# Kernel optimization log

Measured on AMD Instinct MI355X. Metric: run time of the kernel, lower is better.

Reference implementation:

```python
import jax, jax.numpy as jnp
import numpy as np

STRIDES = (8, 16, 32)
IMG = 1024
CENTER_RADIUS = 2.5
N_CAND = 10  # SimOTA candidate top-k


def setup_inputs() -> dict:
    key = jax.random.key(0)
    ks = jax.random.split(key, 6)
    B, G = 16, 100
    sizes = [IMG // s for s in STRIDES]
    inp = {}
    for i, H in enumerate(sizes):
        inp[f"reg{i}"] = jax.random.normal(ks[i], (B, 4, H, H), jnp.float32)
        inp[f"obj{i}"] = jax.random.normal(ks[3 + i], (B, 1, H, H), jnp.float32)
    rng = np.random.default_rng(0)
    cxy = rng.uniform(64.0, IMG - 64.0, (B, G, 2))
    wh = rng.uniform(16.0, 160.0, (B, G, 2))
    labels = np.concatenate([np.zeros((B, G, 1)), cxy, wh], axis=-1).astype(np.float32)
    counts = rng.integers(20, G + 1, B)  # variable num_gt per image, zero-padded tail
    mask = (np.arange(G)[None, :] < counts[:, None]).astype(np.float32)
    labels = labels * mask[:, :, None]
    inp["labels"] = jnp.asarray(labels)
    return inp


def _decode(regs, objs):
    outs, xs, ys, ss = [], [], [], []
    for reg, obj, s in zip(regs, objs, STRIDES):
        B, _, H, W = reg.shape
        o = jnp.concatenate([reg, obj], axis=1).transpose(0, 2, 3, 1).reshape(B, H * W, 5)
        yv, xv = jnp.meshgrid(jnp.arange(H), jnp.arange(W), indexing="ij")
        grid = jnp.stack([xv, yv], axis=-1).reshape(-1, 2).astype(o.dtype)  # [HW,2] (x,y)
        xy = (o[..., :2] + grid) * s
        wh = jnp.exp(o[..., 2:4]) * s
        outs.append(jnp.concatenate([xy, wh, o[..., 4:5]], axis=-1))
        xs.append(grid[:, 0])
        ys.append(grid[:, 1])
        ss.append(jnp.full((H * W,), float(s), o.dtype))
    return (jnp.concatenate(outs, 1), jnp.concatenate(xs), jnp.concatenate(ys), jnp.concatenate(ss))


def _pairwise_iou(gt, pr):
    # gt [G,4], pr [A,4] in cxcywh -> [G,A]
    tl = jnp.maximum(gt[:, None, :2] - gt[:, None, 2:] * 0.5, pr[None, :, :2] - pr[None, :, 2:] * 0.5)
    br = jnp.minimum(gt[:, None, :2] + gt[:, None, 2:] * 0.5, pr[None, :, :2] + pr[None, :, 2:] * 0.5)
    en = jnp.all(tl < br, axis=-1)
    area_i = jnp.prod(br - tl, axis=-1) * en
    area_g = gt[:, 2] * gt[:, 3]
    area_p = pr[:, 2] * pr[:, 3]
    return area_i / (area_g[:, None] + area_p[None, :] - area_i + 1e-16)


def _iou_loss(pred, tgt):
    # elementwise cxcywh IoU loss: 1 - iou**2 (loss_type='iou')
    tl = jnp.maximum(pred[..., :2] - pred[..., 2:] * 0.5, tgt[..., :2] - tgt[..., 2:] * 0.5)
    br = jnp.minimum(pred[..., :2] + pred[..., 2:] * 0.5, tgt[..., :2] + tgt[..., 2:] * 0.5)
    en = jnp.all(tl < br, axis=-1)
    area_i = jnp.prod(br - tl, axis=-1) * en
    area_p = pred[..., 2] * pred[..., 3]
    area_g = tgt[..., 2] * tgt[..., 3]
    iou = area_i / (area_p + area_g - area_i + 1e-16)
    return 1.0 - iou ** 2


def _assign(gt_boxes, gt_valid, bbox, obj_logit, x_c, y_c, strides):
    # SimOTA assignment for one image. gt_boxes [G,4], bbox [A,4].
    G = gt_boxes.shape[0]
    gx, gy, gw, gh = gt_boxes[:, 0], gt_boxes[:, 1], gt_boxes[:, 2], gt_boxes[:, 3]
    bl = x_c[None] - (gx - 0.5 * gw)[:, None]
    br_ = (gx + 0.5 * gw)[:, None] - x_c[None]
    bt = y_c[None] - (gy - 0.5 * gh)[:, None]
    bb = (gy + 0.5 * gh)[:, None] - y_c[None]
    in_boxes = jnp.minimum(jnp.minimum(bl, br_), jnp.minimum(bt, bb)) > 0
    r = CENTER_RADIUS * strides[None]
    cl = x_c[None] - (gx[:, None] - r)
    cr = (gx[:, None] + r) - x_c[None]
    ct = y_c[None] - (gy[:, None] - r)
    cb = (gy[:, None] + r) - y_c[None]
    in_centers = jnp.minimum(jnp.minimum(cl, cr), jnp.minimum(ct, cb)) > 0
    fg_anchor = jnp.any(in_boxes, 0) | jnp.any(in_centers, 0)
    in_both = in_boxes & in_centers

    ious = _pairwise_iou(gt_boxes, bbox)                       # [G,A]
    valid_pair = gt_valid[:, None] & fg_anchor[None, :]
    ious_m = jnp.where(valid_pair, ious, 0.0)
    obj_cost = jax.nn.softplus(-obj_logit)[None, :]            # BCE-with-logits, target=1
    cost = (obj_cost + 3.0 * (-jnp.log(ious + 1e-8))
            + 1e5 * (~in_both) + 1e7 * (~valid_pair))

    topk_ious = jax.lax.top_k(ious_m, N_CAND)[0]               # [G,10]
    dyn_k = jnp.maximum(topk_ious.sum(1).astype(jnp.int32), 1)  # dynamic k per gt
    ranks = jnp.argsort(jnp.argsort(cost, axis=1), axis=1)      # rank of each anchor per gt
    matching = (ranks < dyn_k[:, None]) & gt_valid[:, None]
    n_match = matching.sum(0)
    best_gt = jnp.argmin(cost, axis=0)                          # conflict resolution
    resolved = (jnp.arange(G)[:, None] == best_gt[None, :]) & gt_valid[:, None]
    matching = jnp.where(n_match[None, :] > 1, resolved, matching)
    fg = jnp.any(matching, 0)
    matched_gt = jnp.argmax(matching, 0)
    return fg, matched_gt, fg.sum()


def reference(reg0, reg1, reg2, obj0, obj1, obj2, labels):
    out, x_sh, y_sh, strides = _decode((reg0, reg1, reg2), (obj0, obj1, obj2))
    bbox = out[..., :4]          # [B,A,4] decoded cxcywh
    obj_logit = out[..., 4]      # [B,A]
    x_c = (x_sh + 0.5) * strides
    y_c = (y_sh + 0.5) * strides
    gt_boxes = labels[..., 1:5]
    gt_valid = labels.sum(-1) > 0
    fg, matched_gt, nfg = jax.vmap(_assign, in_axes=(0, 0, 0, 0, None, None, None))(
        gt_boxes, gt_valid, bbox, obj_logit, x_c, y_c, strides)
    num_fg = jnp.maximum(nfg.sum().astype(jnp.float32), 1.0)
    reg_tgt = jax.vmap(lambda g, i: g[i])(gt_boxes, matched_gt)  # [B,A,4]
    fgf = fg.astype(jnp.float32)
    loss_iou = (_iou_loss(bbox, reg_tgt) * fgf).sum() / num_fg
    bce = jax.nn.softplus(obj_logit) - obj_logit * fgf           # BCEWithLogits
    loss_obj = bce.sum() / num_fg
    num_gts = jnp.maximum(gt_valid.sum().astype(jnp.float32), 1.0)
    loss = 5.0 * loss_iou + loss_obj
    return (loss, 5.0 * loss_iou, loss_obj, jnp.float32(0.0), num_fg / num_gts)
```

## Files before the change

kernel.cpp:

```cpp
#include <hip/hip_runtime.h>
#include <math.h>

#define NA   21504
#define NA0  16384
#define NA01 20480
#define NG   100
#define NB   16
#define NC   10
#define NCHK 84
#define NBLK 1344
#define MAXC 192
#define MCAP 1024
#define MSTRIDE 64
#define NSQ  4

__device__ __forceinline__ float softplusf(float x) {
    return fmaxf(x, 0.f) + log1pf(expf(-fabsf(x)));
}

__device__ __forceinline__ unsigned int fmono(float f) {
    unsigned int u = __float_as_uint(f);
    return (f < 0.f) ? ~u : (u | 0x80000000u);
}

__global__ __launch_bounds__(256) void k_decode(
    const float* __restrict__ reg0, const float* __restrict__ obj0,
    const float* __restrict__ reg1, const float* __restrict__ obj1,
    const float* __restrict__ reg2, const float* __restrict__ obj2,
    const float* __restrict__ labels,
    float4* __restrict__ A0, float* __restrict__ OC,
    int* __restrict__ cidx, int* __restrict__ bcnt,
    int* __restrict__ n_match, int* __restrict__ mg_min,
    float* __restrict__ pSp, int* __restrict__ mcount,
    unsigned long long* __restrict__ bestkey, int* __restrict__ fbflag)
{
    int b  = blockIdx.y;
    int bx = blockIdx.x;
    int tid = threadIdx.x;
    int a = bx * 256 + tid;

    int W, ry0, rows; float s;
    if (bx < 64)      { W = 128; s = 8.f;  ry0 = bx * 2;        rows = 2; }
    else if (bx < 80) { W = 64;  s = 16.f; ry0 = (bx - 64) * 4; rows = 4; }
    else              { W = 32;  s = 32.f; ry0 = (bx - 80) * 8; rows = 8; }

    __shared__ unsigned int smask[8];
    if (tid < 8) smask[tid] = 0u;
    __syncthreads();

    if (tid < NG) {
        const float* L = labels + (b * NG + tid) * 5;
        float gx = L[1], gy = L[2], gw = L[3], gh = L[4];
        float r = 2.5f * s;
        float tlx = gx - 0.5f * gw, tly = gy - 0.5f * gh;
        float brx = gx + 0.5f * gw, bry = gy + 0.5f * gh;
        float cxl = gx - r, cxh = gx + r, cyl = gy - r, cyh = gy + r;
        float lox = fminf(tlx, cxl), hix = fmaxf(brx, cxh);
        float loy = fminf(tly, cyl), hiy = fmaxf(bry, cyh);
        int ixA = (int)floorf(lox / s - 0.5f) - 1;
        int ixB = (int)ceilf (hix / s - 0.5f) + 1;
        int iyA = (int)floorf(loy / s - 0.5f) - 1;
        int iyB = (int)ceilf (hiy / s - 0.5f) + 1;
        ixA = max(ixA, 0); ixB = min(ixB, W - 1);
        iyA = max(iyA, ry0); iyB = min(iyB, ry0 + rows - 1);
        for (int iy = iyA; iy <= iyB; iy++) {
            float yc = ((float)iy + 0.5f) * s;
            float mb = fminf(yc - tly, bry - yc);
            float mc = fminf(yc - cyl, cyh - yc);
            for (int ix = ixA; ix <= ixB; ix++) {
                float xc = ((float)ix + 0.5f) * s;
                bool inb = fminf(fminf(xc - tlx, brx - xc), mb) > 0.f;
                bool inc = fminf(fminf(xc - cxl, cxh - xc), mc) > 0.f;
                if (inb || inc) {
                    int bit = (iy - ry0) * W + ix;
                    atomicOr(&smask[bit >> 5], 1u << (bit & 31));
                }
            }
        }
    }

    int x, y, hw, loc;
    const float* regp; const float* objp;
    if (a < NA0)       { x = a & 127;           y = a >> 7; hw = 16384; loc = y * 128 + x; regp = reg0; objp = obj0; }
    else if (a < NA01) { int i = a - NA0;  x = i & 63; y = i >> 6; hw = 4096;  loc = y * 64 + x;  regp = reg1; objp = obj1; }
    else               { int i = a - NA01; x = i & 31; y = i >> 5; hw = 1024;  loc = y * 32 + x;  regp = reg2; objp = obj2; }

    float r0 = regp[(b * 4 + 0) * hw + loc];
    float r1 = regp[(b * 4 + 1) * hw + loc];
    float r2 = regp[(b * 4 + 2) * hw + loc];
    float r3 = regp[(b * 4 + 3) * hw + loc];
    float ol = objp[b * hw + loc];

    float px = (r0 + (float)x) * s, py = (r1 + (float)y) * s;
    float pw = expf(r2) * s,        ph = expf(r3) * s;
    float ocv = softplusf(-ol);

    int idx = b * NA + a;
    A0[idx] = make_float4(px - 0.5f * pw, py - 0.5f * ph, px + 0.5f * pw, py + 0.5f * ph);
    OC[idx] = ocv;
    n_match[idx] = 0;
    mg_min[idx]  = 0x7fffffff;
    bestkey[idx] = 0xFFFFFFFFFFFFFFFFull;

    __syncthreads();
    bool fga = (smask[tid >> 5] >> (tid & 31)) & 1u;

    float sp = ocv + ol;
    for (int off = 32; off > 0; off >>= 1) sp += __shfl_down(sp, off);

    unsigned long long mask = __ballot(fga);
    int lane = tid & 63, wid = tid >> 6;
    __shared__ float wSp[4];
    __shared__ int   wcnt[4];
    if (lane == 0) { wSp[wid] = sp; wcnt[wid] = __popcll(mask); }
    __syncthreads();
    int wbase = 0;
    #pragma unroll
    for (int w2 = 0; w2 < 4; w2++) if (w2 < wid) wbase += wcnt[w2];
    if (fga) {
        int prefix = __popcll(mask & ((1ull << lane) - 1ull));
        cidx[b * NA + bx * 256 + wbase + prefix] = a;
    }
    if (tid == 0) {
        bcnt[b * NCHK + bx] = wcnt[0] + wcnt[1] + wcnt[2] + wcnt[3];
        pSp[b * NCHK + bx]  = wSp[0] + wSp[1] + wSp[2] + wSp[3];
        if (bx == 0) { mcount[b * MSTRIDE] = 0; fbflag[b] = 0; }
    }
}

__global__ __launch_bounds__(256) void k_pack(
    const float4* __restrict__ A0, const float* __restrict__ OC,
    const int* __restrict__ cidx, const int* __restrict__ bcnt,
    float4* __restrict__ PK0, float* __restrict__ PKO, int* __restrict__ PKA,
    int* __restrict__ fcnt)
{
    int b = blockIdx.y, bx = blockIdx.x, tid = threadIdx.x;
    int v = 0;
    for (int i = tid; i < bx; i += 256) v += bcnt[b * NCHK + i];
    for (int off = 32; off > 0; off >>= 1) v += __shfl_down(v, off);
    __shared__ int ws[4];
    int wid = tid >> 6;
    if ((tid & 63) == 0) ws[wid] = v;
    __syncthreads();
    int base = ws[0] + ws[1] + ws[2] + ws[3];
    int nt = bcnt[b * NCHK + bx];
    if (tid < nt) {
        int a = cidx[b * NA + bx * 256 + tid];
        int idx = b * NA + a;
        int d = b * NA + base + tid;
        PK0[d] = A0[idx];
        PKO[d] = OC[idx];
        PKA[d] = a;
    }
    if (bx == NCHK - 1 && tid == 0) fcnt[b] = base + nt;
}

__global__ __launch_bounds__(256) void k_assign(
    const float* __restrict__ labels, const float4* __restrict__ A0,
    const float* __restrict__ OC,
    const float4* __restrict__ PK0, const float* __restrict__ PKO,
    const int* __restrict__ PKA, const int* __restrict__ fcnt,
    int* __restrict__ n_match, int* __restrict__ mg_min,
    int* __restrict__ mlist, int* __restrict__ mcount,
    unsigned long long* __restrict__ bestkey, int* __restrict__ fbflag)
{
    int blk = blockIdx.x;
    int b = blk / NG, g = blk % NG;
    const float* L = labels + (b * NG + g) * 5;
    float l0 = L[0], gx = L[1], gy = L[2], gw = L[3], gh = L[4];
    bool gv = (l0 + gx + gy + gw + gh) > 0.f;
    if (!gv) return;
    int tid = threadIdx.x;

    float g_tlx = gx - 0.5f * gw, g_tly = gy - 0.5f * gh;
    float g_brx = gx + 0.5f * gw, g_bry = gy + 0.5f * gh;
    float ag = gw * gh;
    int bbase = b * NA;

    __shared__ float sio[256 * NC];
    __shared__ int   si2[256 * NC];
    __shared__ int   cand_a[MAXC];
    __shared__ float cand_c[MAXC];
    __shared__ int   scnt;
    if (tid == 0) scnt = 0;
    __syncthreads();

    int cnt = fcnt[b];

    float tio[NC];
    #pragma unroll
    for (int k = 0; k < NC; k++) tio[k] = 0.f;

    for (int m = tid; m < cnt; m += 256) {
        float4 c0 = PK0[bbase + m];
        float pa = (c0.z - c0.x) * (c0.w - c0.y);
        float tlx = fmaxf(g_tlx, c0.x), tly = fmaxf(g_tly, c0.y);
        float brx = fminf(g_brx, c0.z), bry = fminf(g_bry, c0.w);
        bool en = (tlx < brx) && (tly < bry);
        float ai = en ? (brx - tlx) * (bry - tly) : 0.f;
        float iou = ai / (ag + pa - ai + 1e-16f);
        if (iou > tio[NC - 1]) {
            tio[NC - 1] = iou;
            #pragma unroll
            for (int j = NC - 1; j > 0; --j) {
                if (tio[j] > tio[j - 1]) { float t = tio[j]; tio[j] = tio[j - 1]; tio[j - 1] = t; }
            }
        }
    }

    #pragma unroll
    for (int k = 0; k < NC; k++) sio[tid * NC + k] = tio[k];
    __syncthreads();

    for (int off = 128; off > 0; off >>= 1) {
        if (tid < off) {
            int abase = tid * NC, bb2 = (tid + off) * NC;
            int i = 0, j = 0;
            float oo_[NC];
            #pragma unroll
            for (int k = 0; k < NC; k++) {
                float va = sio[abase + i], vb = sio[bb2 + j];
                bool ta = va >= vb;
                oo_[k] = ta ? va : vb;
                i += ta ? 1 : 0; j += ta ? 0 : 1;
            }
            #pragma unroll
            for (int k = 0; k < NC; k++) sio[abase + k] = oo_[k];
        }
        __syncthreads();
    }

    float s10 = 0.f;
    #pragma unroll
    for (int k = 0; k < NC; k++) s10 += sio[k];
    int dk = (int)s10;
    if (dk < 1) dk = 1;
    if (dk > NC) dk = NC;

    for (int lev = 0; lev < 3; lev++) {
        float s  = (lev == 0) ? 8.f : ((lev == 1) ? 16.f : 32.f);
        int   W  = (lev == 0) ? 128 : ((lev == 1) ? 64 : 32);
        int aofs = (lev == 0) ? 0 : ((lev == 1) ? NA0 : NA01);
        float rr = 2.5f * s;
        float gxr_lo = gx - rr, gxr_hi = gx + rr;
        float gyr_lo = gy - rr, gyr_hi = gy + rr;
        float lox = fmaxf(g_tlx, gxr_lo), hix = fminf(g_brx, gxr_hi);
        float loy = fmaxf(g_tly, gyr_lo), hiy = fminf(g_bry, gyr_hi);
        int ixA = (int)floorf(lox / s - 0.5f) - 1;
        int ixB = (int)ceilf (hix / s - 0.5f) + 1;
        int iyA = (int)floorf(loy / s - 0.5f) - 1;
        int iyB = (int)ceilf (hiy / s - 0.5f) + 1;
        ixA = max(ixA, 0); ixB = min(ixB, W - 1);
        iyA = max(iyA, 0); iyB = min(iyB, W - 1);
        int nx = ixB - ixA + 1, ny = iyB - iyA + 1;
        int nt = (nx > 0 && ny > 0) ? nx * ny : 0;
        for (int t = tid; t < nt; t += 256) {
            int ix = ixA + t % nx, iy = iyA + t / nx;
            float xcA = ((float)ix + 0.5f) * s;
            float ycA = ((float)iy + 0.5f) * s;
            float bl = xcA - g_tlx, brr = g_brx - xcA;
            float bt = ycA - g_tly, bbb = g_bry - ycA;
            bool inb = fminf(fminf(bl, brr), fminf(bt, bbb)) > 0.f;
            float cl = xcA - gxr_lo, cr = gxr_hi - xcA;
            float ct = ycA - gyr_lo, cb = gyr_hi - ycA;
            bool inc = fminf(fminf(cl, cr), fminf(ct, cb)) > 0.f;
            if (inb && inc) {
                int p = atomicAdd(&scnt, 1);
                if (p < MAXC) cand_a[p] = aofs + iy * W + ix;
            }
        }
    }
    __syncthreads();
    int nc_ = min(scnt, MAXC);

    if (dk <= nc_) {
        for (int ci = tid; ci < nc_; ci += 256) {
            int a = cand_a[ci];
            float4 c0 = A0[bbase + a];
            float pa = (c0.z - c0.x) * (c0.w - c0.y);
            float tlx = fmaxf(g_tlx, c0.x), tly = fmaxf(g_tly, c0.y);
            float brx = fminf(g_brx, c0.z), bry = fminf(g_bry, c0.w);
            bool en = (tlx < brx) && (tly < bry);
            float ai = en ? (brx - tlx) * (bry - tly) : 0.f;
            float iou = ai / (ag + pa - ai + 1e-16f);
            float c = OC[bbase + a] + 3.0f * (-__logf(iou + 1e-8f));
            cand_c[ci] = c;
            unsigned long long key = ((unsigned long long)fmono(c) << 32) | (unsigned int)g;
            atomicMin(&bestkey[bbase + a], key);
        }
        __syncthreads();
        for (int ci = tid; ci < nc_; ci += 256) {
            float c = cand_c[ci]; int a = cand_a[ci];
            int rank = 0;
            for (int j = 0; j < nc_; j++) {
                float cj = cand_c[j]; int aj = cand_a[j];
                rank += (cj < c || (cj == c && aj < a)) ? 1 : 0;
            }
            if (rank < dk) {
                if (atomicAdd(&n_match[bbase + a], 1) == 0) {
                    int p = atomicAdd(&mcount[b * MSTRIDE], 1);
                    mlist[b * MCAP + p] = a;
                }
                atomicMin(&mg_min[bbase + a], g);
            }
        }
    } else {
        if (tid == 0) fbflag[b] = 1;
        float fc[NC]; int fa[NC];
        #pragma unroll
        for (int k = 0; k < NC; k++) { fc[k] = 3.4e38f; fa[k] = 0x7fffffff; }
        for (int m = tid; m < cnt; m += 256) {
            int a = PKA[bbase + m];
            float4 c0 = PK0[bbase + m];
            float pa = (c0.z - c0.x) * (c0.w - c0.y);
            float tlx = fmaxf(g_tlx, c0.x), tly = fmaxf(g_tly, c0.y);
            float brx = fminf(g_brx, c0.z), bry = fminf(g_bry, c0.w);
            bool en = (tlx < brx) && (tly < bry);
            float ai = en ? (brx - tlx) * (bry - tly) : 0.f;
            float iou = ai / (ag + pa - ai + 1e-16f);
            int xx, yy; float s2;
            if (a < NA0)       { xx = a & 127;           yy = a >> 7;  s2 = 8.f;  }
            else if (a < NA01) { int i2 = a - NA0;  xx = i2 & 63; yy = i2 >> 6; s2 = 16.f; }
            else               { int i2 = a - NA01; xx = i2 & 31; yy = i2 >> 5; s2 = 32.f; }
            float xcA = ((float)xx + 0.5f) * s2, ycA = ((float)yy + 0.5f) * s2;
            float rr2 = 2.5f * s2;
            float bl = xcA - g_tlx, brr = g_brx - xcA;
            float bt = ycA - g_tly, bbb = g_bry - ycA;
            bool inb = fminf(fminf(bl, brr), fminf(bt, bbb)) > 0.f;
            float cl = xcA - (gx - rr2), cr = (gx + rr2) - xcA;
            float ct = ycA - (gy - rr2), cb = (gy + rr2) - ycA;
            bool inc = fminf(fminf(cl, cr), fminf(ct, cb)) > 0.f;
            float c = PKO[bbase + m] + 3.0f * (-__logf(iou + 1e-8f));
            if (!(inb && inc)) c += 100000.0f;
            if (c < fc[NC - 1] || (c == fc[NC - 1] && a < fa[NC - 1])) {
                fc[NC - 1] = c; fa[NC - 1] = a;
                #pragma unroll
                for (int j = NC - 1; j > 0; --j) {
                    bool sw = (fc[j] < fc[j - 1]) || (fc[j] == fc[j - 1] && fa[j] < fa[j - 1]);
                    if (sw) {
                        float t1 = fc[j]; fc[j] = fc[j - 1]; fc[j - 1] = t1;
                        int   t2 = fa[j]; fa[j] = fa[j - 1]; fa[j - 1] = t2;
                    }
                }
            }
        }
        __syncthreads();
        #pragma unroll
        for (int k = 0; k < NC; k++) { sio[tid * NC + k] = fc[k]; si2[tid * NC + k] = fa[k]; }
        __syncthreads();
        for (int off = 128; off > 0; off >>= 1) {
            if (tid < off) {
                int abase = tid * NC, bb2 = (tid + off) * NC;
                int i = 0, j = 0;
                float oc_[NC]; int oi_[NC];
                #pragma unroll
                for (int k = 0; k < NC; k++) {
                    float ca = sio[abase + i], cb3 = sio[bb2 + j];
                    int   ia = si2[abase + i], ib  = si2[bb2 + j];
                    bool ta = (ca < cb3) || (ca == cb3 && ia <= ib);
                    oc_[k] = ta ? ca : cb3; oi_[k] = ta ? ia : ib;
                    i += ta ? 1 : 0; j += ta ? 0 : 1;
                }
                #pragma unroll
                for (int k = 0; k < NC; k++) { sio[abase + k] = oc_[k]; si2[abase + k] = oi_[k]; }
            }
            __syncthreads();
        }
        if (tid == 0) {
            for (int k = 0; k < dk; k++) {
                int aa = si2[k];
                if (aa != 0x7fffffff) {
                    if (atomicAdd(&n_match[bbase + aa], 1) == 0) {
                        int p = atomicAdd(&mcount[b * MSTRIDE], 1);
                        mlist[b * MCAP + p] = aa;
                    }
                    atomicMin(&mg_min[bbase + aa], g);
                }
            }
        }
    }
}

__global__ __launch_bounds__(256) void k_sparse(
    const float* __restrict__ labels,
    const float* __restrict__ obj0, const float* __restrict__ obj1,
    const float* __restrict__ obj2,
    const float4* __restrict__ A0, const float* __restrict__ OC,
    const int* __restrict__ n_match, const int* __restrict__ mg_min,
    const int* __restrict__ mlist, const int* __restrict__ mcount,
    const unsigned long long* __restrict__ bestkey, const int* __restrict__ fbflag,
    float* __restrict__ pIl2, float* __restrict__ pOl, int* __restrict__ pNf2)
{
    int q = blockIdx.x;
    int b = blockIdx.y;
    int tid = threadIdx.x;
    __shared__ float lbl[NG * 5];
    for (int i = tid; i < NG * 5; i += 256) lbl[i] = labels[b * NG * 5 + i];
    __syncthreads();

    int cm = min(mcount[b * MSTRIDE], MCAP);
    int fb = fbflag[b];
    float il_s = 0.f, ol_s = 0.f; int nf = 0;

    for (int m = q * 256 + tid; m < cm; m += NSQ * 256) {
        int a = mlist[b * MCAP + m];
        int idx = b * NA + a;
        int n = n_match[idx];

        int x, y, hw, loc; const float* objp; float s, rr;
        if (a < NA0)       { x = a & 127;            y = a >> 7;  hw = 16384; loc = y * 128 + x; objp = obj0; s = 8.f;  rr = 20.f; }
        else if (a < NA01) { int i2 = a - NA0;  x = i2 & 63; y = i2 >> 6; hw = 4096; loc = y * 64 + x; objp = obj1; s = 16.f; rr = 40.f; }
        else               { int i2 = a - NA01; x = i2 & 31; y = i2 >> 5; hw = 1024; loc = y * 32 + x; objp = obj2; s = 32.f; rr = 80.f; }

        float4 c0 = A0[idx];
        bool fg = false; int mg = 0;
        if (n == 1) { fg = true; mg = mg_min[idx]; }
        else {
            unsigned long long key = fb ? 0xFFFFFFFFFFFFFFFFull : bestkey[idx];
            if (key != 0xFFFFFFFFFFFFFFFFull) {
                fg = true; mg = (int)(key & 0xFFFFFFFFull);
            } else {
                float pa = (c0.z - c0.x) * (c0.w - c0.y);
                float oc = OC[idx];
                float xcA = ((float)x + 0.5f) * s, ycA = ((float)y + 0.5f) * s;
                float bestc = 3.4e38f; int bg = 0;
                for (int g = 0; g < NG; g++) {
                    float l0 = lbl[g * 5 + 0], gx = lbl[g * 5 + 1], gy = lbl[g * 5 + 2];
                    float gw = lbl[g * 5 + 3], gh = lbl[g * 5 + 4];
                    bool gvv = (l0 + gx + gy + gw + gh) > 0.f;
                    float tlx = fmaxf(gx - 0.5f * gw, c0.x), tly = fmaxf(gy - 0.5f * gh, c0.y);
                    float brx = fminf(gx + 0.5f * gw, c0.z), bry = fminf(gy + 0.5f * gh, c0.w);
                    bool en = (tlx < brx) && (tly < bry);
                    float ai = en ? (brx - tlx) * (bry - tly) : 0.f;
                    float iou = ai / (gw * gh + pa - ai + 1e-16f);
                    float bl = xcA - (gx - 0.5f * gw), br = (gx + 0.5f * gw) - xcA;
                    float bt = ycA - (gy - 0.5f * gh), bb = (gy + 0.5f * gh) - ycA;
                    bool inb = fminf(fminf(bl, br), fminf(bt, bb)) > 0.f;
                    float cl = xcA - (gx - rr), cr = (gx + rr) - xcA;
                    float ct = ycA - (gy - rr), cb = (gy + rr) - ycA;
                    bool inc = fminf(fminf(cl, cr), fminf(ct, cb)) > 0.f;
                    float c = oc + 3.0f * (-__logf(iou + 1e-8f));
                    if (!(inb && inc)) c += 100000.0f;
                    if (!gvv)          c += 10000000.0f;
                    if (c < bestc) { bestc = c; bg = g; }
                }
                bool gvv = (lbl[bg * 5 + 0] + lbl[bg * 5 + 1] + lbl[bg * 5 + 2] +
                            lbl[bg * 5 + 3] + lbl[bg * 5 + 4]) > 0.f;
                if (gvv) { fg = true; mg = bg; }
            }
        }

        if (fg) {
            float pa = (c0.z - c0.x) * (c0.w - c0.y);
            float gx = lbl[mg * 5 + 1], gy = lbl[mg * 5 + 2];
            float gw = lbl[mg * 5 + 3], gh = lbl[mg * 5 + 4];
            float tlx = fmaxf(c0.x, gx - 0.5f * gw);
            float tly = fmaxf(c0.y, gy - 0.5f * gh);
            float brx = fminf(c0.z, gx + 0.5f * gw);
            float bry = fminf(c0.w, gy + 0.5f * gh);
            bool en = (tlx < brx) && (tly < bry);
            float ai = en ? (brx - tlx) * (bry - tly) : 0.f;
            float iou = ai / (pa + gw * gh - ai + 1e-16f);
            il_s += 1.f - iou * iou;
            ol_s += objp[b * hw + loc];
            nf++;
        }
    }

    for (int off = 32; off > 0; off >>= 1) {
        il_s += __shfl_down(il_s, off);
        ol_s += __shfl_down(ol_s, off);
        nf   += __shfl_down(nf, off);
    }
    __shared__ float wI[4], wO[4];
    __shared__ int   wN[4];
    int wid = tid >> 6;
    if ((tid & 63) == 0) { wI[wid] = il_s; wO[wid] = ol_s; wN[wid] = nf; }
    __syncthreads();
    if (tid == 0) {
        int pb = b * NSQ + q;
        pIl2[pb] = wI[0] + wI[1] + wI[2] + wI[3];
        pOl[pb]  = wO[0] + wO[1] + wO[2] + wO[3];
        pNf2[pb] = wN[0] + wN[1] + wN[2] + wN[3];
    }
}

__global__ __launch_bounds__(256) void k_fin(
    const float* __restrict__ pSp, const float* __restrict__ pIl2,
    const float* __restrict__ pOl, const int* __restrict__ pNf2,
    const float* __restrict__ labels, float* __restrict__ out)
{
    int tid = threadIdx.x;
    double dSp = 0.0;
    for (int i = tid; i < NBLK; i += 256) dSp += (double)pSp[i];
    double dIl = 0.0, dOl = 0.0; int nf = 0;
    for (int i = tid; i < NB * NSQ; i += 256) {
        dIl += (double)pIl2[i];
        dOl += (double)pOl[i];
        nf  += pNf2[i];
    }
    int ng = 0;
    for (int i = tid; i < NB * NG; i += 256) {
        const float* L = labels + i * 5;
        if (L[0] + L[1] + L[2] + L[3] + L[4] > 0.f) ng++;
    }
    for (int off = 32; off > 0; off >>= 1) {
        dSp += __shfl_down(dSp, off);
        dIl += __shfl_down(dIl, off);
        dOl += __shfl_down(dOl, off);
        nf  += __shfl_down(nf, off);
        ng  += __shfl_down(ng, off);
    }
    __shared__ double sSp[4], sIl[4], sOl[4];
    __shared__ int sNf[4], sNg[4];
    int wid = tid >> 6;
    if ((tid & 63) == 0) { sSp[wid] = dSp; sIl[wid] = dIl; sOl[wid] = dOl; sNf[wid] = nf; sNg[wid] = ng; }
    __syncthreads();
    if (tid == 0) {
        double tSp = sSp[0] + sSp[1] + sSp[2] + sSp[3];
        double tIl = sIl[0] + sIl[1] + sIl[2] + sIl[3];
        double tOl = sOl[0] + sOl[1] + sOl[2] + sOl[3];
        int tNf = sNf[0] + sNf[1] + sNf[2] + sNf[3];
        int tNg = sNg[0] + sNg[1] + sNg[2] + sNg[3];
        float num_fg  = fmaxf((float)tNf, 1.f);
        float num_gts = fmaxf((float)tNg, 1.f);
        float li = (float)(tIl / (double)num_fg);
        float lo = (float)((tSp - tOl) / (double)num_fg);
        out[0] = 5.f * li + lo;
        out[1] = 5.f * li;
        out[2] = lo;
        out[3] = 0.f;
        out[4] = num_fg / num_gts;
    }
}

extern "C" void kernel_launch(void* const* d_in, const int* in_sizes, int n_in,
                              void* d_out, int out_size, void* d_ws, size_t ws_size,
                              hipStream_t stream)
{
    const float* reg0   = (const float*)d_in[0];
    const float* obj0   = (const float*)d_in[1];
    const float* reg1   = (const float*)d_in[2];
    const float* obj1   = (const float*)d_in[3];
    const float* reg2   = (const float*)d_in[4];
    const float* obj2   = (const float*)d_in[5];
    const float* labels = (const float*)d_in[6];
    float* out = (float*)d_out;

    char* w = (char*)d_ws;
    size_t off = 0;
    int*    mcount = (int*)(w + off);     off += (size_t)NB * MSTRIDE * 4;
    int*    bcnt   = (int*)(w + off);     off += (size_t)NB * NCHK * 4;
    int*    fcnt   = (int*)(w + off);     off += (size_t)NB * 4;
    int*    fbflag = (int*)(w + off);     off += (size_t)NB * 4;
    float*  pSp    = (float*)(w + off);   off += (size_t)NBLK * 4;
    float*  pIl2   = (float*)(w + off);   off += (size_t)NB * NSQ * 4;
    float*  pOl    = (float*)(w + off);   off += (size_t)NB * NSQ * 4;
    int*    pNf2   = (int*)(w + off);     off += (size_t)NB * NSQ * 4;
    off = (off + 255) & ~(size_t)255;
    float4* A0      = (float4*)(w + off); off += (size_t)NB * NA * 16;
    float4* PK0     = (float4*)(w + off); off += (size_t)NB * NA * 16;
    unsigned long long* bestkey = (unsigned long long*)(w + off); off += (size_t)NB * NA * 8;
    float*  OC      = (float*)(w + off);  off += (size_t)NB * NA * 4;
    float*  PKO     = (float*)(w + off);  off += (size_t)NB * NA * 4;
    int*    PKA     = (int*)(w + off);    off += (size_t)NB * NA * 4;
    int*    cidx    = (int*)(w + off);    off += (size_t)NB * NA * 4;
    int*    n_match = (int*)(w + off);    off += (size_t)NB * NA * 4;
    int*    mg_min  = (int*)(w + off);    off += (size_t)NB * NA * 4;
    int*    mlist   = (int*)(w + off);    off += (size_t)NB * MCAP * 4;

    dim3 gA(NCHK, NB);

    k_decode<<<gA, 256, 0, stream>>>(reg0, obj0, reg1, obj1, reg2, obj2, labels,
                                     A0, OC, cidx, bcnt, n_match, mg_min, pSp, mcount,
                                     bestkey, fbflag);
    k_pack<<<gA, 256, 0, stream>>>(A0, OC, cidx, bcnt, PK0, PKO, PKA, fcnt);
    k_assign<<<dim3(NB * NG), 256, 0, stream>>>(labels, A0, OC, PK0, PKO, PKA, fcnt,
                                                n_match, mg_min, mlist, mcount,
                                                bestkey, fbflag);
    k_sparse<<<dim3(NSQ, NB), 256, 0, stream>>>(labels, obj0, obj1, obj2, A0, OC,
                                                n_match, mg_min, mlist, mcount,
                                                bestkey, fbflag, pIl2, pOl, pNf2);
    k_fin<<<1, 256, 0, stream>>>(pSp, pIl2, pOl, pNf2, labels, out);
}
```

Baseline: 123.8 us.

## Fuse sparse loss and final reduction into assign kernel via last-block counters

Folds the k_sparse and k_fin stages into k_assign. Per-image done counters let the last gt block of each image run the loss accumulation, and a global counter lets the last image block compute the final output. Decode now writes boxes and objectness cost only for anchors that pass the centre/box prefilter, and the per-anchor state initialisation moves into the pack kernel, which only touches candidate anchors. The aim is to cut two kernel launches and a large share of global writes. In exchange it adds a memset, atomic fences and serial tail work on one block per image.

```diff
diff --git a/kernel.cpp b/kernel.cpp
--- a/kernel.cpp
+++ b/kernel.cpp
@@ -12,7 +12,7 @@
 #define MAXC 192
 #define MCAP 1024
 #define MSTRIDE 64
-#define NSQ  4
+#define DSTRIDE 64
 
 __device__ __forceinline__ float softplusf(float x) {
     return fmaxf(x, 0.f) + log1pf(expf(-fabsf(x)));
@@ -30,9 +30,7 @@
     const float* __restrict__ labels,
     float4* __restrict__ A0, float* __restrict__ OC,
     int* __restrict__ cidx, int* __restrict__ bcnt,
-    int* __restrict__ n_match, int* __restrict__ mg_min,
-    float* __restrict__ pSp, int* __restrict__ mcount,
-    unsigned long long* __restrict__ bestkey, int* __restrict__ fbflag)
+    float* __restrict__ pSp)
 {
     int b  = blockIdx.y;
     int bx = blockIdx.x;
@@ -95,15 +93,14 @@
     float pw = expf(r2) * s,        ph = expf(r3) * s;
     float ocv = softplusf(-ol);
 
-    int idx = b * NA + a;
-    A0[idx] = make_float4(px - 0.5f * pw, py - 0.5f * ph, px + 0.5f * pw, py + 0.5f * ph);
-    OC[idx] = ocv;
-    n_match[idx] = 0;
-    mg_min[idx]  = 0x7fffffff;
-    bestkey[idx] = 0xFFFFFFFFFFFFFFFFull;
-
     __syncthreads();
     bool fga = (smask[tid >> 5] >> (tid & 31)) & 1u;
+
+    int idx = b * NA + a;
+    if (fga) {
+        A0[idx] = make_float4(px - 0.5f * pw, py - 0.5f * ph, px + 0.5f * pw, py + 0.5f * ph);
+        OC[idx] = ocv;
+    }
 
     float sp = ocv + ol;
     for (int off = 32; off > 0; off >>= 1) sp += __shfl_down(sp, off);
@@ -124,7 +121,6 @@
     if (tid == 0) {
         bcnt[b * NCHK + bx] = wcnt[0] + wcnt[1] + wcnt[2] + wcnt[3];
         pSp[b * NCHK + bx]  = wSp[0] + wSp[1] + wSp[2] + wSp[3];
-        if (bx == 0) { mcount[b * MSTRIDE] = 0; fbflag[b] = 0; }
     }
 }
 
@@ -132,7 +128,10 @@
     const float4* __restrict__ A0, const float* __restrict__ OC,
     const int* __restrict__ cidx, const int* __restrict__ bcnt,
     float4* __restrict__ PK0, float* __restrict__ PKO, int* __restrict__ PKA,
-    int* __restrict__ fcnt)
+    int* __restrict__ fcnt,
+    int* __restrict__ n_match, int* __restrict__ mg_min,
+    unsigned long long* __restrict__ bestkey,
+    int* __restrict__ mcount, int* __restrict__ fbflag)
 {
     int b = blockIdx.y, bx = blockIdx.x, tid = threadIdx.x;
     int v = 0;
@@ -151,166 +150,59 @@
         PK0[d] = A0[idx];
         PKO[d] = OC[idx];
         PKA[d] = a;
+        n_match[idx] = 0;
+        mg_min[idx]  = 0x7fffffff;
+        bestkey[idx] = 0xFFFFFFFFFFFFFFFFull;
     }
     if (bx == NCHK - 1 && tid == 0) fcnt[b] = base + nt;
+    if (bx == 0 && tid == 0) { mcount[b * MSTRIDE] = 0; fbflag[b] = 0; }
 }
 
 __global__ __launch_bounds__(256) void k_assign(
     const float* __restrict__ labels, const float4* __restrict__ A0,
     const float* __restrict__ OC,
+    const float* __restrict__ obj0, const float* __restrict__ obj1,
+    const float* __restrict__ obj2,
     const float4* __restrict__ PK0, const float* __restrict__ PKO,
     const int* __restrict__ PKA, const int* __restrict__ fcnt,
     int* __restrict__ n_match, int* __restrict__ mg_min,
     int* __restrict__ mlist, int* __restrict__ mcount,
-    unsigned long long* __restrict__ bestkey, int* __restrict__ fbflag)
+    unsigned long long* __restrict__ bestkey, int* __restrict__ fbflag,
+    const float* __restrict__ pSp,
+    float* __restrict__ pIl2, float* __restrict__ pOl, int* __restrict__ pNf2,
+    int* __restrict__ doneA, int* __restrict__ gdone,
+    float* __restrict__ out)
 {
     int blk = blockIdx.x;
     int b = blk / NG, g = blk % NG;
-    const float* L = labels + (b * NG + g) * 5;
-    float l0 = L[0], gx = L[1], gy = L[2], gw = L[3], gh = L[4];
-    bool gv = (l0 + gx + gy + gw + gh) > 0.f;
-    if (!gv) return;
     int tid = threadIdx.x;
-
-    float g_tlx = gx - 0.5f * gw, g_tly = gy - 0.5f * gh;
-    float g_brx = gx + 0.5f * gw, g_bry = gy + 0.5f * gh;
-    float ag = gw * gh;
-    int bbase = b * NA;
 
     __shared__ float sio[256 * NC];
     __shared__ int   si2[256 * NC];
     __shared__ int   cand_a[MAXC];
     __shared__ float cand_c[MAXC];
     __shared__ int   scnt;
-    if (tid == 0) scnt = 0;
-    __syncthreads();
-
-    int cnt = fcnt[b];
-
-    float tio[NC];
-    #pragma unroll
-    for (int k = 0; k < NC; k++) tio[k] = 0.f;
-
-    for (int m = tid; m < cnt; m += 256) {
-        float4 c0 = PK0[bbase + m];
-        float pa = (c0.z - c0.x) * (c0.w - c0.y);
-        float tlx = fmaxf(g_tlx, c0.x), tly = fmaxf(g_tly, c0.y);
-        float brx = fminf(g_brx, c0.z), bry = fminf(g_bry, c0.w);
-        bool en = (tlx < brx) && (tly < bry);
-        float ai = en ? (brx - tlx) * (bry - tly) : 0.f;
-        float iou = ai / (ag + pa - ai + 1e-16f);
-        if (iou > tio[NC - 1]) {
-            tio[NC - 1] = iou;
-            #pragma unroll
-            for (int j = NC - 1; j > 0; --j) {
-                if (tio[j] > tio[j - 1]) { float t = tio[j]; tio[j] = tio[j - 1]; tio[j - 1] = t; }
-            }
-        }
-    }
-
-    #pragma unroll
-    for (int k = 0; k < NC; k++) sio[tid * NC + k] = tio[k];
-    __syncthreads();
-
-    for (int off = 128; off > 0; off >>= 1) {
-        if (tid < off) {
-            int abase = tid * NC, bb2 = (tid + off) * NC;
-            int i = 0, j = 0;
-            float oo_[NC];
-            #pragma unroll
-            for (int k = 0; k < NC; k++) {
-                float va = sio[abase + i], vb = sio[bb2 + j];
-                bool ta = va >= vb;
-                oo_[k] = ta ? va : vb;
-                i += ta ? 1 : 0; j += ta ? 0 : 1;
-            }
-            #pragma unroll
-            for (int k = 0; k < NC; k++) sio[abase + k] = oo_[k];
-        }
+    __shared__ int   s_t, s_g;
+
+    const float* L = labels + (b * NG + g) * 5;
+    float l0 = L[0], gx = L[1], gy = L[2], gw = L[3], gh = L[4];
+    bool gv = (l0 + gx + gy + gw + gh) > 0.f;
+    int bbase = b * NA;
+
+    if (gv) {
+        float g_tlx = gx - 0.5f * gw, g_tly = gy - 0.5f * gh;
+        float g_brx = gx + 0.5f * gw, g_bry = gy + 0.5f * gh;
+        float ag = gw * gh;
+        if (tid == 0) scnt = 0;
         __syncthreads();
-    }
-
-    float s10 = 0.f;
-    #pragma unroll
-    for (int k = 0; k < NC; k++) s10 += sio[k];
-    int dk = (int)s10;
-    if (dk < 1) dk = 1;
-    if (dk > NC) dk = NC;
-
-    for (int lev = 0; lev < 3; lev++) {
-        float s  = (lev == 0) ? 8.f : ((lev == 1) ? 16.f : 32.f);
-        int   W  = (lev == 0) ? 128 : ((lev == 1) ? 64 : 32);
-        int aofs = (lev == 0) ? 0 : ((lev == 1) ? NA0 : NA01);
-        float rr = 2.5f * s;
-        float gxr_lo = gx - rr, gxr_hi = gx + rr;
-        float gyr_lo = gy - rr, gyr_hi = gy + rr;
-        float lox = fmaxf(g_tlx, gxr_lo), hix = fminf(g_brx, gxr_hi);
-        float loy = fmaxf(g_tly, gyr_lo), hiy = fminf(g_bry, gyr_hi);
-        int ixA = (int)floorf(lox / s - 0.5f) - 1;
-        int ixB = (int)ceilf (hix / s - 0.5f) + 1;
-        int iyA = (int)floorf(loy / s - 0.5f) - 1;
-        int iyB = (int)ceilf (hiy / s - 0.5f) + 1;
-        ixA = max(ixA, 0); ixB = min(ixB, W - 1);
-        iyA = max(iyA, 0); iyB = min(iyB, W - 1);
-        int nx = ixB - ixA + 1, ny = iyB - iyA + 1;
-        int nt = (nx > 0 && ny > 0) ? nx * ny : 0;
-        for (int t = tid; t < nt; t += 256) {
-            int ix = ixA + t % nx, iy = iyA + t / nx;
-            float xcA = ((float)ix + 0.5f) * s;
-            float ycA = ((float)iy + 0.5f) * s;
-            float bl = xcA - g_tlx, brr = g_brx - xcA;
-            float bt = ycA - g_tly, bbb = g_bry - ycA;
-            bool inb = fminf(fminf(bl, brr), fminf(bt, bbb)) > 0.f;
-            float cl = xcA - gxr_lo, cr = gxr_hi - xcA;
-            float ct = ycA - gyr_lo, cb = gyr_hi - ycA;
-            bool inc = fminf(fminf(cl, cr), fminf(ct, cb)) > 0.f;
-            if (inb && inc) {
-                int p = atomicAdd(&scnt, 1);
-                if (p < MAXC) cand_a[p] = aofs + iy * W + ix;
-            }
-        }
-    }
-    __syncthreads();
-    int nc_ = min(scnt, MAXC);
-
-    if (dk <= nc_) {
-        for (int ci = tid; ci < nc_; ci += 256) {
-            int a = cand_a[ci];
-            float4 c0 = A0[bbase + a];
-            float pa = (c0.z - c0.x) * (c0.w - c0.y);
-            float tlx = fmaxf(g_tlx, c0.x), tly = fmaxf(g_tly, c0.y);
-            float brx = fminf(g_brx, c0.z), bry = fminf(g_bry, c0.w);
-            bool en = (tlx < brx) && (tly < bry);
-            float ai = en ? (brx - tlx) * (bry - tly) : 0.f;
-            float iou = ai / (ag + pa - ai + 1e-16f);
-            float c = OC[bbase + a] + 3.0f * (-__logf(iou + 1e-8f));
-            cand_c[ci] = c;
-            unsigned long long key = ((unsigned long long)fmono(c) << 32) | (unsigned int)g;
-            atomicMin(&bestkey[bbase + a], key);
-        }
-        __syncthreads();
-        for (int ci = tid; ci < nc_; ci += 256) {
-            float c = cand_c[ci]; int a = cand_a[ci];
-            int rank = 0;
-            for (int j = 0; j < nc_; j++) {
-                float cj = cand_c[j]; int aj = cand_a[j];
-                rank += (cj < c || (cj == c && aj < a)) ? 1 : 0;
-            }
-            if (rank < dk) {
-                if (atomicAdd(&n_match[bbase + a], 1) == 0) {
-                    int p = atomicAdd(&mcount[b * MSTRIDE], 1);
-                    mlist[b * MCAP + p] = a;
-                }
-                atomicMin(&mg_min[bbase + a], g);
-            }
-        }
-    } else {
-        if (tid == 0) fbflag[b] = 1;
-        float fc[NC]; int fa[NC];
+
+        int cnt = fcnt[b];
+
+        float tio[NC];
         #pragma unroll
-        for (int k = 0; k < NC; k++) { fc[k] = 3.4e38f; fa[k] = 0x7fffffff; }
+        for (int k = 0; k < NC; k++) tio[k] = 0.f;
+
         for (int m = tid; m < cnt; m += 256) {
-            int a = PKA[bbase + m];
             float4 c0 = PK0[bbase + m];
             float pa = (c0.z - c0.x) * (c0.w - c0.y);
             float tlx = fmaxf(g_tlx, c0.x), tly = fmaxf(g_tly, c0.y);
@@ -318,219 +210,329 @@
             bool en = (tlx < brx) && (tly < bry);
             float ai = en ? (brx - tlx) * (bry - tly) : 0.f;
             float iou = ai / (ag + pa - ai + 1e-16f);
-            int xx, yy; float s2;
-            if (a < NA0)       { xx = a & 127;           yy = a >> 7;  s2 = 8.f;  }
-            else if (a < NA01) { int i2 = a - NA0;  xx = i2 & 63; yy = i2 >> 6; s2 = 16.f; }
-            else               { int i2 = a - NA01; xx = i2 & 31; yy = i2 >> 5; s2 = 32.f; }
-            float xcA = ((float)xx + 0.5f) * s2, ycA = ((float)yy + 0.5f) * s2;
-            float rr2 = 2.5f * s2;
-            float bl = xcA - g_tlx, brr = g_brx - xcA;
-            float bt = ycA - g_tly, bbb = g_bry - ycA;
-            bool inb = fminf(fminf(bl, brr), fminf(bt, bbb)) > 0.f;
-            float cl = xcA - (gx - rr2), cr = (gx + rr2) - xcA;
-            float ct = ycA - (gy - rr2), cb = (gy + rr2) - ycA;
-            bool inc = fminf(fminf(cl, cr), fminf(ct, cb)) > 0.f;
-            float c = PKO[bbase + m] + 3.0f * (-__logf(iou + 1e-8f));
-            if (!(inb && inc)) c += 100000.0f;
-            if (c < fc[NC - 1] || (c == fc[NC - 1] && a < fa[NC - 1])) {
-                fc[NC - 1] = c; fa[NC - 1] = a;
+            if (iou > tio[NC - 1]) {
+                tio[NC - 1] = iou;
                 #pragma unroll
                 for (int j = NC - 1; j > 0; --j) {
-                    bool sw = (fc[j] < fc[j - 1]) || (fc[j] == fc[j - 1] && fa[j] < fa[j - 1]);
-                    if (sw) {
-                        float t1 = fc[j]; fc[j] = fc[j - 1]; fc[j - 1] = t1;
-                        int   t2 = fa[j]; fa[j] = fa[j - 1]; fa[j - 1] = t2;
-                    }
-                }
-            }
-        }
+                    if (tio[j] > tio[j - 1]) { float t = tio[j]; tio[j] = tio[j - 1]; tio[j - 1] = t; }
+                }
+            }
+        }
+
+        #pragma unroll
+        for (int k = 0; k < NC; k++) sio[tid * NC + k] = tio[k];
         __syncthreads();
-        #pragma unroll
-        for (int k = 0; k < NC; k++) { sio[tid * NC + k] = fc[k]; si2[tid * NC + k] = fa[k]; }
-        __syncthreads();
+
         for (int off = 128; off > 0; off >>= 1) {
             if (tid < off) {
                 int abase = tid * NC, bb2 = (tid + off) * NC;
                 int i = 0, j = 0;
-                float oc_[NC]; int oi_[NC];
+                float oo_[NC];
                 #pragma unroll
                 for (int k = 0; k < NC; k++) {
-                    float ca = sio[abase + i], cb3 = sio[bb2 + j];
-                    int   ia = si2[abase + i], ib  = si2[bb2 + j];
-                    bool ta = (ca < cb3) || (ca == cb3 && ia <= ib);
-                    oc_[k] = ta ? ca : cb3; oi_[k] = ta ? ia : ib;
+                    float va = sio[abase + i], vb = sio[bb2 + j];
+                    bool ta = va >= vb;
+                    oo_[k] = ta ? va : vb;
                     i += ta ? 1 : 0; j += ta ? 0 : 1;
                 }
                 #pragma unroll
-                for (int k = 0; k < NC; k++) { sio[abase + k] = oc_[k]; si2[abase + k] = oi_[k]; }
+                for (int k = 0; k < NC; k++) sio[abase + k] = oo_[k];
             }
             __syncthreads();
         }
+
+        float s10 = 0.f;
+        #pragma unroll
+        for (int k = 0; k < NC; k++) s10 += sio[k];
+        int dk = (int)s10;
+        if (dk < 1) dk = 1;
+        if (dk > NC) dk = NC;
+
+        for (int lev = 0; lev < 3; lev++) {
+            float s  = (lev == 0) ? 8.f : ((lev == 1) ? 16.f : 32.f);
+            int   W  = (lev == 0) ? 128 : ((lev == 1) ? 64 : 32);
+            int aofs = (lev == 0) ? 0 : ((lev == 1) ? NA0 : NA01);
+            float rr = 2.5f * s;
+            float gxr_lo = gx - rr, gxr_hi = gx + rr;
+            float gyr_lo = gy - rr, gyr_hi = gy + rr;
+            float lox = fmaxf(g_tlx, gxr_lo), hix = fminf(g_brx, gxr_hi);
+            float loy = fmaxf(g_tly, gyr_lo), hiy = fminf(g_bry, gyr_hi);
+            int ixA = (int)floorf(lox / s - 0.5f) - 1;
+            int ixB = (int)ceilf (hix / s - 0.5f) + 1;
+            int iyA = (int)floorf(loy / s - 0.5f) - 1;
+            int iyB = (int)ceilf (hiy / s - 0.5f) + 1;
+            ixA = max(ixA, 0); ixB = min(ixB, W - 1);
+            iyA = max(iyA, 0); iyB = min(iyB, W - 1);
+            int nx = ixB - ixA + 1, ny = iyB - iyA + 1;
+            int nt = (nx > 0 && ny > 0) ? nx * ny : 0;
+            for (int t = tid; t < nt; t += 256) {
+                int ix = ixA + t % nx, iy = iyA + t / nx;
+                float xcA = ((float)ix + 0.5f) * s;
+                float ycA = ((float)iy + 0.5f) * s;
+                float bl = xcA - g_tlx, brr = g_brx - xcA;
+                float bt = ycA - g_tly, bbb = g_bry - ycA;
+                bool inb = fminf(fminf(bl, brr), fminf(bt, bbb)) > 0.f;
+                float cl = xcA - gxr_lo, cr = gxr_hi - xcA;
+                float ct = ycA - gyr_lo, cb = gyr_hi - ycA;
+                bool inc = fminf(fminf(cl, cr), fminf(ct, cb)) > 0.f;
+                if (inb && inc) {
+                    int p = atomicAdd(&scnt, 1);
+                    if (p < MAXC) cand_a[p] = aofs + iy * W + ix;
+                }
+            }
+        }
+        __syncthreads();
+        int nc_ = min(scnt, MAXC);
+
+        if (dk <= nc_) {
+            for (int ci = tid; ci < nc_; ci += 256) {
+                int a = cand_a[ci];
+                float4 c0 = A0[bbase + a];
+                float pa = (c0.z - c0.x) * (c0.w - c0.y);
+                float tlx = fmaxf(g_tlx, c0.x), tly = fmaxf(g_tly, c0.y);
+                float brx = fminf(g_brx, c0.z), bry = fminf(g_bry, c0.w);
+                bool en = (tlx < brx) && (tly < bry);
+                float ai = en ? (brx - tlx) * (bry - tly) : 0.f;
+                float iou = ai / (ag + pa - ai + 1e-16f);
+                float c = OC[bbase + a] + 3.0f * (-__logf(iou + 1e-8f));
+                cand_c[ci] = c;
+                unsigned long long key = ((unsigned long long)fmono(c) << 32) | (unsigned int)g;
+                atomicMin(&bestkey[bbase + a], key);
+            }
+            __syncthreads();
+            for (int ci = tid; ci < nc_; ci += 256) {
+                float c = cand_c[ci]; int a = cand_a[ci];
+                int rank = 0;
+                for (int j = 0; j < nc_; j++) {
+                    float cj = cand_c[j]; int aj = cand_a[j];
+                    rank += (cj < c || (cj == c && aj < a)) ? 1 : 0;
+                }
+                if (rank < dk) {
+                    if (atomicAdd(&n_match[bbase + a], 1) == 0) {
+                        int p = atomicAdd(&mcount[b * MSTRIDE], 1);
+                        atomicExch(&mlist[b * MCAP + p], a);
+                    }
+                    atomicMin(&mg_min[bbase + a], g);
+                }
+            }
+        } else {
+            if (tid == 0) atomicExch(&fbflag[b], 1);
+            int cnt2 = cnt;
+            float fc[NC]; int fa[NC];
+            #pragma unroll
+            for (int k = 0; k < NC; k++) { fc[k] = 3.4e38f; fa[k] = 0x7fffffff; }
+            for (int m = tid; m < cnt2; m += 256) {
+                int a = PKA[bbase + m];
+                float4 c0 = PK0[bbase + m];
+                float pa = (c0.z - c0.x) * (c0.w - c0.y);
+                float tlx = fmaxf(g_tlx, c0.x), tly = fmaxf(g_tly, c0.y);
+                float brx = fminf(g_brx, c0.z), bry = fminf(g_bry, c0.w);
+                bool en = (tlx < brx) && (tly < bry);
+                float ai = en ? (brx - tlx) * (bry - tly) : 0.f;
+                float iou = ai / (ag + pa - ai + 1e-16f);
+                int xx, yy; float s2;
+                if (a < NA0)       { xx = a & 127;           yy = a >> 7;  s2 = 8.f;  }
+                else if (a < NA01) { int i2 = a - NA0;  xx = i2 & 63; yy = i2 >> 6; s2 = 16.f; }
+                else               { int i2 = a - NA01; xx = i2 & 31; yy = i2 >> 5; s2 = 32.f; }
+                float xcA = ((float)xx + 0.5f) * s2, ycA = ((float)yy + 0.5f) * s2;
+                float rr2 = 2.5f * s2;
+                float bl = xcA - g_tlx, brr = g_brx - xcA;
+                float bt = ycA - g_tly, bbb = g_bry - ycA;
+                bool inb = fminf(fminf(bl, brr), fminf(bt, bbb)) > 0.f;
+                float cl = xcA - (gx - rr2), cr = (gx + rr2) - xcA;
+                float ct = ycA - (gy - rr2), cb = (gy + rr2) - ycA;
+                bool inc = fminf(fminf(cl, cr), fminf(ct, cb)) > 0.f;
+                float c = PKO[bbase + m] + 3.0f * (-__logf(iou + 1e-8f));
+                if (!(inb && inc)) c += 100000.0f;
+                if (c < fc[NC - 1] || (c == fc[NC - 1] && a < fa[NC - 1])) {
+                    fc[NC - 1] = c; fa[NC - 1] = a;
+                    #pragma unroll
+                    for (int j = NC - 1; j > 0; --j) {
+                        bool sw = (fc[j] < fc[j - 1]) || (fc[j] == fc[j - 1] && fa[j] < fa[j - 1]);
+                        if (sw) {
+                            float t1 = fc[j]; fc[j] = fc[j - 1]; fc[j - 1] = t1;
+                            int   t2 = fa[j]; fa[j] = fa[j - 1]; fa[j - 1] = t2;
+                        }
+                    }
+                }
+            }
+            __syncthreads();
+            #pragma unroll
+            for (int k = 0; k < NC; k++) { sio[tid * NC + k] = fc[k]; si2[tid * NC + k] = fa[k]; }
+            __syncthreads();
+            for (int off = 128; off > 0; off >>= 1) {
+                if (tid < off) {
+                    int abase = tid * NC, bb2 = (tid + off) * NC;
+                    int i = 0, j = 0;
+                    float oc_[NC]; int oi_[NC];
+                    #pragma unroll
+                    for (int k = 0; k < NC; k++) {
+                        float ca = sio[abase + i], cb3 = sio[bb2 + j];
+                        int   ia = si2[abase + i], ib  = si2[bb2 + j];
+                        bool ta = (ca < cb3) || (ca == cb3 && ia <= ib);
+                        oc_[k] = ta ? ca : cb3; oi_[k] = ta ? ia : ib;
+                        i += ta ? 1 : 0; j += ta ? 0 : 1;
+                    }
+                    #pragma unroll
+                    for (int k = 0; k < NC; k++) { sio[abase + k] = oc_[k]; si2[abase + k] = oi_[k]; }
+                }
+                __syncthreads();
+            }
+            if (tid == 0) {
+                for (int k = 0; k < dk; k++) {
+                    int aa = si2[k];
+                    if (aa != 0x7fffffff) {
+                        if (atomicAdd(&n_match[bbase + aa], 1) == 0) {
+                            int p = atomicAdd(&mcount[b * MSTRIDE], 1);
+                            atomicExch(&mlist[b * MCAP + p], aa);
+                        }
+                        atomicMin(&mg_min[bbase + aa], g);
+                    }
+                }
+            }
+        }
+    }
+
+    __syncthreads();
+    if (tid == 0) s_t = atomicAdd(&doneA[b * DSTRIDE], 1);
+    __syncthreads();
+    if (s_t == NG - 1) {
+        __threadfence();
+        float* lbl = sio;
+        for (int i = tid; i < NG * 5; i += 256) lbl[i] = labels[b * NG * 5 + i];
+        __syncthreads();
+
+        int cm = min(mcount[b * MSTRIDE], MCAP);
+        int fb = fbflag[b];
+        float il_s = 0.f, ol_s = 0.f; int nf = 0;
+
+        for (int m = tid; m < cm; m += 256) {
+            int a = mlist[b * MCAP + m];
+            int idx = bbase + a;
+            int n = n_match[idx];
+
+            int x, y, hw, loc; const float* objp; float s, rr;
+            if (a < NA0)       { x = a & 127;            y = a >> 7;  hw = 16384; loc = y * 128 + x; objp = obj0; s = 8.f;  rr = 20.f; }
+            else if (a < NA01) { int i2 = a - NA0;  x = i2 & 63; y = i2 >> 6; hw = 4096; loc = y * 64 + x; objp = obj1; s = 16.f; rr = 40.f; }
+            else               { int i2 = a - NA01; x = i2 & 31; y = i2 >> 5; hw = 1024; loc = y * 32 + x; objp = obj2; s = 32.f; rr = 80.f; }
+
+            float4 c0 = A0[idx];
+            bool fg = false; int mg = 0;
+            if (n == 1) { fg = true; mg = mg_min[idx]; }
+            else {
+                unsigned long long key = fb ? 0xFFFFFFFFFFFFFFFFull : bestkey[idx];
+                if (key != 0xFFFFFFFFFFFFFFFFull) {
+                    fg = true; mg = (int)(key & 0xFFFFFFFFull);
+                } else {
+                    float pa = (c0.z - c0.x) * (c0.w - c0.y);
+                    float oc = OC[idx];
+                    float xcA = ((float)x + 0.5f) * s, ycA = ((float)y + 0.5f) * s;
+                    float bestc = 3.4e38f; int bg = 0;
+                    for (int g2 = 0; g2 < NG; g2++) {
+                        float l02 = lbl[g2 * 5 + 0], gx2 = lbl[g2 * 5 + 1], gy2 = lbl[g2 * 5 + 2];
+                        float gw2 = lbl[g2 * 5 + 3], gh2 = lbl[g2 * 5 + 4];
+                        bool gvv = (l02 + gx2 + gy2 + gw2 + gh2) > 0.f;
+                        float tlx = fmaxf(gx2 - 0.5f * gw2, c0.x), tly = fmaxf(gy2 - 0.5f * gh2, c0.y);
+                        float brx = fminf(gx2 + 0.5f * gw2, c0.z), bry = fminf(gy2 + 0.5f * gh2, c0.w);
+                        bool en = (tlx < brx) && (tly < bry);
+                        float ai = en ? (brx - tlx) * (bry - tly) : 0.f;
+                        float iou = ai / (gw2 * gh2 + pa - ai + 1e-16f);
+                        float bl = xcA - (gx2 - 0.5f * gw2), br = (gx2 + 0.5f * gw2) - xcA;
+                        float bt = ycA - (gy2 - 0.5f * gh2), bb = (gy2 + 0.5f * gh2) - ycA;
+                        bool inb = fminf(fminf(bl, br), fminf(bt, bb)) > 0.f;
+                        float cl = xcA - (gx2 - rr), cr = (gx2 + rr) - xcA;
+                        float ct = ycA - (gy2 - rr), cb = (gy2 + rr) - ycA;
+                        bool inc = fminf(fminf(cl, cr), fminf(ct, cb)) > 0.f;
+                        float c = oc + 3.0f * (-__logf(iou + 1e-8f));
+                        if (!(inb && inc)) c += 100000.0f;
+                        if (!gvv)          c += 10000000.0f;
+                        if (c < bestc) { bestc = c; bg = g2; }
+                    }
+                    bool gvv = (lbl[bg * 5 + 0] + lbl[bg * 5 + 1] + lbl[bg * 5 + 2] +
+                                lbl[bg * 5 + 3] + lbl[bg * 5 + 4]) > 0.f;
+                    if (gvv) { fg = true; mg = bg; }
+                }
+            }
+
+            if (fg) {
+                float pa = (c0.z - c0.x) * (c0.w - c0.y);
+                float gx2 = lbl[mg * 5 + 1], gy2 = lbl[mg * 5 + 2];
+                float gw2 = lbl[mg * 5 + 3], gh2 = lbl[mg * 5 + 4];
+                float tlx = fmaxf(c0.x, gx2 - 0.5f * gw2);
+                float tly = fmaxf(c0.y, gy2 - 0.5f * gh2);
+                float brx = fminf(c0.z, gx2 + 0.5f * gw2);
+                float bry = fminf(c0.w, gy2 + 0.5f * gh2);
+                bool en = (tlx < brx) && (tly < bry);
+                float ai = en ? (brx - tlx) * (bry - tly) : 0.f;
+                float iou = ai / (pa + gw2 * gh2 - ai + 1e-16f);
+                il_s += 1.f - iou * iou;
+                ol_s += objp[b * hw + loc];
+                nf++;
+            }
+        }
+
+        for (int off = 32; off > 0; off >>= 1) {
+            il_s += __shfl_down(il_s, off);
+            ol_s += __shfl_down(ol_s, off);
+            nf   += __shfl_down(nf, off);
+        }
+        __shared__ float wI[4], wO[4];
+        __shared__ int   wN[4];
+        int wid = tid >> 6;
+        if ((tid & 63) == 0) { wI[wid] = il_s; wO[wid] = ol_s; wN[wid] = nf; }
+        __syncthreads();
         if (tid == 0) {
-            for (int k = 0; k < dk; k++) {
-                int aa = si2[k];
-                if (aa != 0x7fffffff) {
-                    if (atomicAdd(&n_match[bbase + aa], 1) == 0) {
-                        int p = atomicAdd(&mcount[b * MSTRIDE], 1);
-                        mlist[b * MCAP + p] = aa;
-                    }
-                    atomicMin(&mg_min[bbase + aa], g);
-                }
-            }
-        }
-    }
-}
-
-__global__ __launch_bounds__(256) void k_sparse(
-    const float* __restrict__ labels,
-    const float* __restrict__ obj0, const float* __restrict__ obj1,
-    const float* __restrict__ obj2,
-    const float4* __restrict__ A0, const float* __restrict__ OC,
-    const int* __restrict__ n_match, const int* __restrict__ mg_min,
-    const int* __restrict__ mlist, const int* __restrict__ mcount,
-    const unsigned long long* __restrict__ bestkey, const int* __restrict__ fbflag,
-    float* __restrict__ pIl2, float* __restrict__ pOl, int* __restrict__ pNf2)
-{
-    int q = blockIdx.x;
-    int b = blockIdx.y;
-    int tid = threadIdx.x;
-    __shared__ float lbl[NG * 5];
-    for (int i = tid; i < NG * 5; i += 256) lbl[i] = labels[b * NG * 5 + i];
-    __syncthreads();
-
-    int cm = min(mcount[b * MSTRIDE], MCAP);
-    int fb = fbflag[b];
-    float il_s = 0.f, ol_s = 0.f; int nf = 0;
-
-    for (int m = q * 256 + tid; m < cm; m += NSQ * 256) {
-        int a = mlist[b * MCAP + m];
-        int idx = b * NA + a;
-        int n = n_match[idx];
-
-        int x, y, hw, loc; const float* objp; float s, rr;
-        if (a < NA0)       { x = a & 127;            y = a >> 7;  hw = 16384; loc = y * 128 + x; objp = obj0; s = 8.f;  rr = 20.f; }
-        else if (a < NA01) { int i2 = a - NA0;  x = i2 & 63; y = i2 >> 6; hw = 4096; loc = y * 64 + x; objp = obj1; s = 16.f; rr = 40.f; }
-        else               { int i2 = a - NA01; x = i2 & 31; y = i2 >> 5; hw = 1024; loc = y * 32 + x; objp = obj2; s = 32.f; rr = 80.f; }
-
-        float4 c0 = A0[idx];
-        bool fg = false; int mg = 0;
-        if (n == 1) { fg = true; mg = mg_min[idx]; }
-        else {
-            unsigned long long key = fb ? 0xFFFFFFFFFFFFFFFFull : bestkey[idx];
-            if (key != 0xFFFFFFFFFFFFFFFFull) {
-                fg = true; mg = (int)(key & 0xFFFFFFFFull);
-            } else {
-                float pa = (c0.z - c0.x) * (c0.w - c0.y);
-                float oc = OC[idx];
-                float xcA = ((float)x + 0.5f) * s, ycA = ((float)y + 0.5f) * s;
-                float bestc = 3.4e38f; int bg = 0;
-                for (int g = 0; g < NG; g++) {
-                    float l0 = lbl[g * 5 + 0], gx = lbl[g * 5 + 1], gy = lbl[g * 5 + 2];
-                    float gw = lbl[g * 5 + 3], gh = lbl[g * 5 + 4];
-                    bool gvv = (l0 + gx + gy + gw + gh) > 0.f;
-                    float tlx = fmaxf(gx - 0.5f * gw, c0.x), tly = fmaxf(gy - 0.5f * gh, c0.y);
-                    float brx = fminf(gx + 0.5f * gw, c0.z), bry = fminf(gy + 0.5f * gh, c0.w);
-                    bool en = (tlx < brx) && (tly < bry);
-                    float ai = en ? (brx - tlx) * (bry - tly) : 0.f;
-                    float iou = ai / (gw * gh + pa - ai + 1e-16f);
-                    float bl = xcA - (gx - 0.5f * gw), br = (gx + 0.5f * gw) - xcA;
-                    float bt = ycA - (gy - 0.5f * gh), bb = (gy + 0.5f * gh) - ycA;
-                    bool inb = fminf(fminf(bl, br), fminf(bt, bb)) > 0.f;
-                    float cl = xcA - (gx - rr), cr = (gx + rr) - xcA;
-                    float ct = ycA - (gy - rr), cb = (gy + rr) - ycA;
-                    bool inc = fminf(fminf(cl, cr), fminf(ct, cb)) > 0.f;
-                    float c = oc + 3.0f * (-__logf(iou + 1e-8f));
-                    if (!(inb && inc)) c += 100000.0f;
-                    if (!gvv)          c += 10000000.0f;
-                    if (c < bestc) { bestc = c; bg = g; }
-                }
-                bool gvv = (lbl[bg * 5 + 0] + lbl[bg * 5 + 1] + lbl[bg * 5 + 2] +
-                            lbl[bg * 5 + 3] + lbl[bg * 5 + 4]) > 0.f;
-                if (gvv) { fg = true; mg = bg; }
-            }
-        }
-
-        if (fg) {
-            float pa = (c0.z - c0.x) * (c0.w - c0.y);
-            float gx = lbl[mg * 5 + 1], gy = lbl[mg * 5 + 2];
-            float gw = lbl[mg * 5 + 3], gh = lbl[mg * 5 + 4];
-            float tlx = fmaxf(c0.x, gx - 0.5f * gw);
-            float tly = fmaxf(c0.y, gy - 0.5f * gh);
-            float brx = fminf(c0.z, gx + 0.5f * gw);
-            float bry = fminf(c0.w, gy + 0.5f * gh);
-            bool en = (tlx < brx) && (tly < bry);
-            float ai = en ? (brx - tlx) * (bry - tly) : 0.f;
-            float iou = ai / (pa + gw * gh - ai + 1e-16f);
-            il_s += 1.f - iou * iou;
-            ol_s += objp[b * hw + loc];
-            nf++;
-        }
-    }
-
-    for (int off = 32; off > 0; off >>= 1) {
-        il_s += __shfl_down(il_s, off);
-        ol_s += __shfl_down(ol_s, off);
-        nf   += __shfl_down(nf, off);
-    }
-    __shared__ float wI[4], wO[4];
-    __shared__ int   wN[4];
-    int wid = tid >> 6;
-    if ((tid & 63) == 0) { wI[wid] = il_s; wO[wid] = ol_s; wN[wid] = nf; }
-    __syncthreads();
-    if (tid == 0) {
-        int pb = b * NSQ + q;
-        pIl2[pb] = wI[0] + wI[1] + wI[2] + wI[3];
-        pOl[pb]  = wO[0] + wO[1] + wO[2] + wO[3];
-        pNf2[pb] = wN[0] + wN[1] + wN[2] + wN[3];
-    }
-}
-
-__global__ __launch_bounds__(256) void k_fin(
-    const float* __restrict__ pSp, const float* __restrict__ pIl2,
-    const float* __restrict__ pOl, const int* __restrict__ pNf2,
-    const float* __restrict__ labels, float* __restrict__ out)
-{
-    int tid = threadIdx.x;
-    double dSp = 0.0;
-    for (int i = tid; i < NBLK; i += 256) dSp += (double)pSp[i];
-    double dIl = 0.0, dOl = 0.0; int nf = 0;
-    for (int i = tid; i < NB * NSQ; i += 256) {
-        dIl += (double)pIl2[i];
-        dOl += (double)pOl[i];
-        nf  += pNf2[i];
-    }
-    int ng = 0;
-    for (int i = tid; i < NB * NG; i += 256) {
-        const float* L = labels + i * 5;
-        if (L[0] + L[1] + L[2] + L[3] + L[4] > 0.f) ng++;
-    }
-    for (int off = 32; off > 0; off >>= 1) {
-        dSp += __shfl_down(dSp, off);
-        dIl += __shfl_down(dIl, off);
-        dOl += __shfl_down(dOl, off);
-        nf  += __shfl_down(nf, off);
-        ng  += __shfl_down(ng, off);
-    }
-    __shared__ double sSp[4], sIl[4], sOl[4];
-    __shared__ int sNf[4], sNg[4];
-    int wid = tid >> 6;
-    if ((tid & 63) == 0) { sSp[wid] = dSp; sIl[wid] = dIl; sOl[wid] = dOl; sNf[wid] = nf; sNg[wid] = ng; }
-    __syncthreads();
-    if (tid == 0) {
-        double tSp = sSp[0] + sSp[1] + sSp[2] + sSp[3];
-        double tIl = sIl[0] + sIl[1] + sIl[2] + sIl[3];
-        double tOl = sOl[0] + sOl[1] + sOl[2] + sOl[3];
-        int tNf = sNf[0] + sNf[1] + sNf[2] + sNf[3];
-        int tNg = sNg[0] + sNg[1] + sNg[2] + sNg[3];
-        float num_fg  = fmaxf((float)tNf, 1.f);
-        float num_gts = fmaxf((float)tNg, 1.f);
-        float li = (float)(tIl / (double)num_fg);
-        float lo = (float)((tSp - tOl) / (double)num_fg);
-        out[0] = 5.f * li + lo;
-        out[1] = 5.f * li;
-        out[2] = lo;
-        out[3] = 0.f;
-        out[4] = num_fg / num_gts;
+            pIl2[b] = wI[0] + wI[1] + wI[2] + wI[3];
+            pOl[b]  = wO[0] + wO[1] + wO[2] + wO[3];
+            pNf2[b] = wN[0] + wN[1] + wN[2] + wN[3];
+            __threadfence();
+            s_g = atomicAdd(gdone, 1);
+        }
+        __syncthreads();
+
+        if (s_g == NB - 1) {
+            __threadfence();
+            double dSp = 0.0;
+            for (int i = tid; i < NBLK; i += 256) dSp += (double)pSp[i];
+            double dIl = 0.0, dOl = 0.0; int nf2 = 0;
+            if (tid < NB) {
+                dIl = (double)pIl2[tid];
+                dOl = (double)pOl[tid];
+                nf2 = pNf2[tid];
+            }
+            int ng = 0;
+            for (int i = tid; i < NB * NG; i += 256) {
+                const float* L2 = labels + i * 5;
+                if (L2[0] + L2[1] + L2[2] + L2[3] + L2[4] > 0.f) ng++;
+            }
+            for (int off = 32; off > 0; off >>= 1) {
+                dSp += __shfl_down(dSp, off);
+                dIl += __shfl_down(dIl, off);
+                dOl += __shfl_down(dOl, off);
+                nf2 += __shfl_down(nf2, off);
+                ng  += __shfl_down(ng, off);
+            }
+            __shared__ double fSp[4], fIl[4], fOl[4];
+            __shared__ int fNf[4], fNg[4];
+            if ((tid & 63) == 0) { fSp[wid] = dSp; fIl[wid] = dIl; fOl[wid] = dOl; fNf[wid] = nf2; fNg[wid] = ng; }
+            __syncthreads();
+            if (tid == 0) {
+                double tSp = fSp[0] + fSp[1] + fSp[2] + fSp[3];
+                double tIl = fIl[0] + fIl[1] + fIl[2] + fIl[3];
+                double tOl = fOl[0] + fOl[1] + fOl[2] + fOl[3];
+                int tNf = fNf[0] + fNf[1] + fNf[2] + fNf[3];
+                int tNg = fNg[0] + fNg[1] + fNg[2] + fNg[3];
+                float num_fg  = fmaxf((float)tNf, 1.f);
+                float num_gts = fmaxf((float)tNg, 1.f);
+                float li = (float)(tIl / (double)num_fg);
+                float lo = (float)((tSp - tOl) / (double)num_fg);
+                out[0] = 5.f * li + lo;
+                out[1] = 5.f * li;
+                out[2] = lo;
+                out[3] = 0.f;
+                out[4] = num_fg / num_gts;
+            }
+        }
     }
 }
 
@@ -549,14 +551,16 @@
 
     char* w = (char*)d_ws;
     size_t off = 0;
+    int*    doneA  = (int*)(w + off);     off += (size_t)NB * DSTRIDE * 4;
+    int*    gdone  = (int*)(w + off);     off += 256;
     int*    mcount = (int*)(w + off);     off += (size_t)NB * MSTRIDE * 4;
     int*    bcnt   = (int*)(w + off);     off += (size_t)NB * NCHK * 4;
     int*    fcnt   = (int*)(w + off);     off += (size_t)NB * 4;
     int*    fbflag = (int*)(w + off);     off += (size_t)NB * 4;
     float*  pSp    = (float*)(w + off);   off += (size_t)NBLK * 4;
-    float*  pIl2   = (float*)(w + off);   off += (size_t)NB * NSQ * 4;
-    float*  pOl    = (float*)(w + off);   off += (size_t)NB * NSQ * 4;
-    int*    pNf2   = (int*)(w + off);     off += (size_t)NB * NSQ * 4;
+    float*  pIl2   = (float*)(w + off);   off += (size_t)NB * 4;
+    float*  pOl    = (float*)(w + off);   off += (size_t)NB * 4;
+    int*    pNf2   = (int*)(w + off);     off += (size_t)NB * 4;
     off = (off + 255) & ~(size_t)255;
     float4* A0      = (float4*)(w + off); off += (size_t)NB * NA * 16;
     float4* PK0     = (float4*)(w + off); off += (size_t)NB * NA * 16;
@@ -571,15 +575,14 @@
 
     dim3 gA(NCHK, NB);
 
+    hipMemsetAsync(doneA, 0, (size_t)NB * DSTRIDE * 4 + 256, stream);
     k_decode<<<gA, 256, 0, stream>>>(reg0, obj0, reg1, obj1, reg2, obj2, labels,
-                                     A0, OC, cidx, bcnt, n_match, mg_min, pSp, mcount,
-                                     bestkey, fbflag);
-    k_pack<<<gA, 256, 0, stream>>>(A0, OC, cidx, bcnt, PK0, PKO, PKA, fcnt);
-    k_assign<<<dim3(NB * NG), 256, 0, stream>>>(labels, A0, OC, PK0, PKO, PKA, fcnt,
+                                     A0, OC, cidx, bcnt, pSp);
+    k_pack<<<gA, 256, 0, stream>>>(A0, OC, cidx, bcnt, PK0, PKO, PKA, fcnt,
+                                   n_match, mg_min, bestkey, mcount, fbflag);
+    k_assign<<<dim3(NB * NG), 256, 0, stream>>>(labels, A0, OC, obj0, obj1, obj2,
+                                                PK0, PKO, PKA, fcnt,
                                                 n_match, mg_min, mlist, mcount,
-                                                bestkey, fbflag);
-    k_sparse<<<dim3(NSQ, NB), 256, 0, stream>>>(labels, obj0, obj1, obj2, A0, OC,
-                                                n_match, mg_min, mlist, mcount,
-                                                bestkey, fbflag, pIl2, pOl, pNf2);
-    k_fin<<<1, 256, 0, stream>>>(pSp, pIl2, pOl, pNf2, labels, out);
+                                                bestkey, fbflag, pSp,
+                                                pIl2, pOl, pNf2, doneA, gdone, out);
 }
```

Result: slower. 128.9 us (+4.1%).
